# Kernel tuning notes

Measured on AMD Instinct MI355X. Metric: run time of the kernel, lower is better.

Reference implementation:

```python
import jax, jax.numpy as jnp
import numpy as np

N, E = 50000, 1600000            # nodes, edges
IN, H, OUT = 128, 128, 64        # in_channels, hidden_channels, out_channels
EPS = 1e-5                       # BatchNorm eps


def setup_inputs() -> dict:
    key = jax.random.key(0)
    ks = jax.random.split(key, 9)
    glorot = lambda k, shp, fan: jax.random.normal(k, shp, jnp.float32) * (1.0 / np.sqrt(fan))
    return {
        "x": jax.random.normal(ks[0], (N, IN), jnp.float32),
        "edge_index": jax.random.randint(ks[1], (2, E), 0, N),
        # layer 0: SAGEConv(IN, H) + BatchNorm(H)
        "Wl0": glorot(ks[2], (H, IN), IN), "Wr0": glorot(ks[3], (H, IN), IN),
        "b0": jnp.zeros((H,), jnp.float32),
        "g0": jnp.ones((H,), jnp.float32), "be0": jnp.zeros((H,), jnp.float32),
        # layer 1: SAGEConv(H, H) + BatchNorm(H)
        "Wl1": glorot(ks[4], (H, H), H), "Wr1": glorot(ks[5], (H, H), H),
        "b1": jnp.zeros((H,), jnp.float32),
        "g1": jnp.ones((H,), jnp.float32), "be1": jnp.zeros((H,), jnp.float32),
        # layer 2: SAGEConv(H, OUT)
        "Wl2": glorot(ks[6], (OUT, H), H), "Wr2": glorot(ks[7], (OUT, H), H),
        "b2": jnp.zeros((OUT,), jnp.float32),
    }


def _sage_conv(x, src, dst, Wl, Wr, b):
    """PyG SAGEConv with mean aggregation: lin_l(mean_{j->i} x_j) + lin_r(x_i) + b."""
    deg = jax.ops.segment_sum(jnp.ones((src.shape[0],), x.dtype), dst, num_segments=N)
    agg = jax.ops.segment_sum(x[src], dst, num_segments=N)  # [N, d] scatter-sum of gathered msgs
    agg = agg / jnp.maximum(deg, 1.0)[:, None]              # scatter-mean (0 for isolated nodes)
    return agg @ Wl.T + x @ Wr.T + b


def _batchnorm(x, gamma, beta):
    # training-mode BN over the node dimension (batch statistics)
    mu = jnp.mean(x, axis=0)
    var = jnp.var(x, axis=0)
    return (x - mu) * jax.lax.rsqrt(var + EPS) * gamma + beta


def reference(x, edge_index, Wl0, Wr0, b0, g0, be0, Wl1, Wr1, b1, g1, be1, Wl2, Wr2, b2):
    src, dst = edge_index[0], edge_index[1]
    h = jax.nn.relu(_batchnorm(_sage_conv(x, src, dst, Wl0, Wr0, b0), g0, be0))
    h = jax.nn.relu(_batchnorm(_sage_conv(h, src, dst, Wl1, Wr1, b1), g1, be1))
    return _sage_conv(h, src, dst, Wl2, Wr2, b2)
```

## Files before the change

### kernel.cpp

```cpp
#include <hip/hip_runtime.h>

#define NND 50000
#define NED 1600000
#define EPSBN 1e-5f
#define NB 196
#define EPB 8192
#define SCELEM (NB * NB)
#define SCPAD (38 * 1024)

typedef __attribute__((ext_vector_type(8))) short short8;
typedef __attribute__((ext_vector_type(4))) float f32x4;

__device__ __forceinline__ float bf_lo(unsigned u) {
    union { unsigned u; float f; } c; c.u = u << 16; return c.f;
}
__device__ __forceinline__ float bf_hi(unsigned u) {
    union { unsigned u; float f; } c; c.u = u & 0xffff0000u; return c.f;
}
__device__ __forceinline__ unsigned short f2b(float f) {
    union { float f; unsigned u; } c; c.f = f;
    unsigned r = (c.u + 0x7fffu + ((c.u >> 16) & 1u)) >> 16;
    return (unsigned short)r;
}

__global__ __launch_bounds__(256) void cast_bf16_kernel(const float* __restrict__ x,
                                                        unsigned short* __restrict__ xb) {
    int i = blockIdx.x * 256 + threadIdx.x;
    if (i >= NND * 16) return;
    const float4* p = (const float4*)x + (size_t)i * 2;
    float4 a = p[0], b = p[1];
    uint4 o;
    o.x = f2b(a.x) | ((unsigned)f2b(a.y) << 16);
    o.y = f2b(a.z) | ((unsigned)f2b(a.w) << 16);
    o.z = f2b(b.x) | ((unsigned)f2b(b.y) << 16);
    o.w = f2b(b.z) | ((unsigned)f2b(b.w) << 16);
    ((uint4*)xb)[i] = o;
}

__global__ __launch_bounds__(256) void eb_hist_kernel(const int* __restrict__ dst,
                                                      int* __restrict__ cntT) {
    __shared__ int hs[256];
    int t = threadIdx.x;
    hs[t] = 0;
    if (blockIdx.x == 0) {
        for (int i = t; i < SCPAD - SCELEM; i += 256) cntT[SCELEM + i] = 0;
    }
    __syncthreads();
    int base = blockIdx.x * EPB;
    for (int i = t; i < EPB; i += 256) {
        int e = base + i;
        if (e < NED) atomicAdd(&hs[dst[e] >> 8], 1);
    }
    __syncthreads();
    if (t < NB) cntT[t * NB + blockIdx.x] = hs[t];
}

__global__ __launch_bounds__(1024) void scan_p1_kernel(int* __restrict__ cnt,
                                                       int* __restrict__ psum) {
    __shared__ int s[1024];
    int t = threadIdx.x;
    int idx = blockIdx.x * 1024 + t;
    int v = cnt[idx];
    s[t] = v;
    __syncthreads();
    for (int o = 1; o < 1024; o <<= 1) {
        int a = (t >= o) ? s[t - o] : 0;
        __syncthreads();
        s[t] += a;
        __syncthreads();
    }
    cnt[idx] = s[t] - v;
    if (t == 1023) psum[blockIdx.x] = s[t];
}

__global__ __launch_bounds__(64) void scan_p2_kernel(int* __restrict__ psum,
                                                     int* __restrict__ binOff,
                                                     int* __restrict__ rowptr) {
    __shared__ int s[64];
    int t = threadIdx.x;
    int v = (t < 38) ? psum[t] : 0;
    s[t] = v;
    __syncthreads();
    for (int o = 1; o < 64; o <<= 1) {
        int a = (t >= o) ? s[t - o] : 0;
        __syncthreads();
        s[t] += a;
        __syncthreads();
    }
    if (t < 38) psum[t] = s[t] - v;
    if (t == 0) { binOff[NB] = NED; rowptr[NND] = NED; }
}

__global__ __launch_bounds__(1024) void scan_p3_kernel(int* __restrict__ cnt,
                                                       const int* __restrict__ psum,
                                                       int* __restrict__ binOff) {
    int idx = blockIdx.x * 1024 + threadIdx.x;
    int val = cnt[idx] + psum[blockIdx.x];
    cnt[idx] = val;
    int bin = idx / NB;
    if (bin < NB && idx - bin * NB == 0) binOff[bin] = val;
}

__global__ __launch_bounds__(256) void eb_scatter_kernel(const int* __restrict__ src,
                                                         const int* __restrict__ dst,
                                                         const int* __restrict__ offT,
                                                         unsigned* __restrict__ pairs) {
    __shared__ int cur[256];
    int t = threadIdx.x;
    if (t < NB) cur[t] = offT[t * NB + blockIdx.x];
    __syncthreads();
    int base = blockIdx.x * EPB;
    for (int i = t; i < EPB; i += 256) {
        int e = base + i;
        if (e < NED) {
            int d = dst[e];
            int pos = atomicAdd(&cur[d >> 8], 1);
            pairs[pos] = ((unsigned)src[e] << 8) | (unsigned)(d & 255);
        }
    }
}

__global__ __launch_bounds__(256) void bucket_finalize_kernel(const unsigned* __restrict__ pairs,
                                                              const int* __restrict__ binOff,
                                                              int* __restrict__ rowptr,
                                                              float* __restrict__ dinv,
                                                              int* __restrict__ csr) {
    __shared__ int hist[256], s[256], cur[256];
    int b = blockIdx.x, t = threadIdx.x;
    int beg = binOff[b], end = binOff[b + 1];
    hist[t] = 0;
    __syncthreads();
    for (int e = beg + t; e < end; e += 256)
        atomicAdd(&hist[pairs[e] & 255u], 1);
    __syncthreads();
    int v = hist[t];
    s[t] = v;
    __syncthreads();
#pragma unroll
    for (int o = 1; o < 256; o <<= 1) {
        int a = (t >= o) ? s[t - o] : 0;
        __syncthreads();
        s[t] += a;
        __syncthreads();
    }
    int base = beg + s[t] - v;
    int node = b * 256 + t;
    if (node < NND) {
        rowptr[node] = base;
        dinv[node] = 1.0f / (float)(v > 1 ? v : 1);
    }
    cur[t] = base;
    __syncthreads();
    for (int e = beg + t; e < end; e += 256) {
        unsigned p = pairs[e];
        int pos = atomicAdd(&cur[p & 255u], 1);
        csr[pos] = (int)(p >> 8);
    }
}

__global__ __launch_bounds__(256) void gather128_kernel(const unsigned short* __restrict__ xb,
                                                        const int* __restrict__ rowptr,
                                                        const int* __restrict__ csr,
                                                        const float* __restrict__ dinv,
                                                        unsigned short* __restrict__ aggb) {
    int w = threadIdx.x >> 6;
    int node = blockIdx.x * 4 + w;
    if (node >= NND) return;
    int lane = threadIdx.x & 63;
    int q = lane >> 4;
    int c8 = lane & 15;
    int beg = rowptr[node], end = rowptr[node + 1];
    const uint4* xv = (const uint4*)xb;

    float acc[8];
#pragma unroll
    for (int i = 0; i < 8; ++i) acc[i] = 0.f;

    for (int j = beg + q; j < end; j += 4) {
        int s = csr[j];
        uint4 v = xv[(size_t)s * 16 + c8];
        acc[0] += bf_lo(v.x); acc[1] += bf_hi(v.x);
        acc[2] += bf_lo(v.y); acc[3] += bf_hi(v.y);
        acc[4] += bf_lo(v.z); acc[5] += bf_hi(v.z);
        acc[6] += bf_lo(v.w); acc[7] += bf_hi(v.w);
    }
#pragma unroll
    for (int i = 0; i < 8; ++i) {
        acc[i] += __shfl_xor(acc[i], 16);
        acc[i] += __shfl_xor(acc[i], 32);
    }
    if (q == 0) {
        float dv = dinv[node];
        uint4 o;
        o.x = f2b(acc[0] * dv) | ((unsigned)f2b(acc[1] * dv) << 16);
        o.y = f2b(acc[2] * dv) | ((unsigned)f2b(acc[3] * dv) << 16);
        o.z = f2b(acc[4] * dv) | ((unsigned)f2b(acc[5] * dv) << 16);
        o.w = f2b(acc[6] * dv) | ((unsigned)f2b(acc[7] * dv) << 16);
        ((uint4*)aggb)[(size_t)node * 16 + c8] = o;
    }
}

__global__ __launch_bounds__(256) void gather64_kernel(const unsigned short* __restrict__ tb,
                                                       const int* __restrict__ rowptr,
                                                       const int* __restrict__ csr,
                                                       const float* __restrict__ dinv,
                                                       float* __restrict__ out) {
    int w = threadIdx.x >> 6;
    int node = blockIdx.x * 4 + w;
    if (node >= NND) return;
    int lane = threadIdx.x & 63;
    int g = lane >> 3;
    int c8 = lane & 7;
    int beg = rowptr[node], end = rowptr[node + 1];
    const uint4* tv = (const uint4*)tb;

    float acc[8];
#pragma unroll
    for (int i = 0; i < 8; ++i) acc[i] = 0.f;

    for (int j = beg + g; j < end; j += 8) {
        int s = csr[j];
        uint4 v = tv[(size_t)s * 8 + c8];
        acc[0] += bf_lo(v.x); acc[1] += bf_hi(v.x);
        acc[2] += bf_lo(v.y); acc[3] += bf_hi(v.y);
        acc[4] += bf_lo(v.z); acc[5] += bf_hi(v.z);
        acc[6] += bf_lo(v.w); acc[7] += bf_hi(v.w);
    }
#pragma unroll
    for (int i = 0; i < 8; ++i) {
        acc[i] += __shfl_xor(acc[i], 8);
        acc[i] += __shfl_xor(acc[i], 16);
        acc[i] += __shfl_xor(acc[i], 32);
    }
    if (g == 0) {
        float dv = dinv[node];
        float* po = out + (size_t)node * 64 + c8 * 8;
        float4 a = *(float4*)po, b = *(float4*)(po + 4);
        a.x += acc[0] * dv; a.y += acc[1] * dv; a.z += acc[2] * dv; a.w += acc[3] * dv;
        b.x += acc[4] * dv; b.y += acc[5] * dv; b.z += acc[6] * dv; b.w += acc[7] * dv;
        *(float4*)po = a; *(float4*)(po + 4) = b;
    }
}

__global__ __launch_bounds__(256) void pack_all_kernel(const float* __restrict__ Wl0,
                                                       const float* __restrict__ Wr0,
                                                       const float* __restrict__ Wl1,
                                                       const float* __restrict__ Wr1,
                                                       const float* __restrict__ Wl2,
                                                       const float* __restrict__ Wr2,
                                                       unsigned short* __restrict__ wp0,
                                                       unsigned short* __restrict__ wp1,
                                                       unsigned short* __restrict__ wp2,
                                                       float* __restrict__ stats) {
    int blk = blockIdx.x;
    if (blk == 0) { stats[threadIdx.x] = 0.f; stats[256 + threadIdx.x] = 0.f; }
    const float *Wl, *Wr; unsigned short* wp; bool l2f; int t;
    if (blk < 16)      { Wl = Wl0; Wr = Wr0; wp = wp0; l2f = false; t = blk * 256 + threadIdx.x; }
    else if (blk < 32) { Wl = Wl1; Wr = Wr1; wp = wp1; l2f = false; t = (blk - 16) * 256 + threadIdx.x; }
    else               { Wl = Wl2; Wr = Wr2; wp = wp2; l2f = true;  t = (blk - 32) * 256 + threadIdx.x; }
    int rem = t & 511;
    int ks = t >> 9;
    int cf = rem >> 6, l = rem & 63;
    int c = cf * 16 + (l & 15);
    int kb = ks * 32 + ((l >> 4) * 8);
    unsigned short v[8];
#pragma unroll
    for (int j = 0; j < 8; ++j) {
        int k = kb + j;
        float w;
        if (l2f) w = (c < 64) ? Wl[c * 128 + k] : Wr[(c - 64) * 128 + k];
        else     w = (k < 128) ? Wl[c * 128 + k] : Wr[c * 128 + (k - 128)];
        v[j] = f2b(w);
    }
    uint4 o;
    o.x = v[0] | ((unsigned)v[1] << 16);
    o.y = v[2] | ((unsigned)v[3] << 16);
    o.z = v[4] | ((unsigned)v[5] << 16);
    o.w = v[6] | ((unsigned)v[7] << 16);
    ((uint4*)wp)[t] = o;
}

template<int KS, int MODE>
__global__ __launch_bounds__(256) void gemm_mfma_kernel(const unsigned short* __restrict__ aggb,
                                                        const unsigned short* xinb,
                                                        const unsigned short* __restrict__ wpack,
                                                        const float* __restrict__ bias,
                                                        void* outv,
                                                        unsigned short* __restrict__ tbuf,
                                                        float* __restrict__ stats) {
    constexpr int NCF = 8, NCOL = 128;
    constexpr bool ST = (MODE == 0);
    __shared__ float o_s[64][NCOL + 4];
    __shared__ float sum_s[ST ? 4 : 1][ST ? 128 : 1];
    __shared__ float sq_s[ST ? 4 : 1][ST ? 128 : 1];

    const int t = threadIdx.x, wave = t >> 6, lane = t & 63;
    const int row0 = blockIdx.x * 64;
    const int arow = row0 + wave * 16 + (lane & 15);
    const bool avalid = arow < NND;
    const int ko = (lane >> 4) * 8;

    f32x4 acc[NCF];
#pragma unroll
    for (int cf = 0; cf < NCF; ++cf) acc[cf] = (f32x4){0.f, 0.f, 0.f, 0.f};

    const short8* wp = (const short8*)wpack;
#pragma unroll
    for (int ks = 0; ks < KS; ++ks) {
        short8 a = {0, 0, 0, 0, 0, 0, 0, 0};
        if (avalid) {
            int k = ks * 32 + ko;
            const unsigned short* base;
            if (MODE == 0)
                base = (k < 128) ? (aggb + (size_t)arow * 128 + k)
                                 : (xinb + (size_t)arow * 128 + (k - 128));
            else
                base = xinb + (size_t)arow * 128 + k;
            a = *(const short8*)base;
        }
#pragma unroll
        for (int cf = 0; cf < NCF; ++cf) {
            short8 b = wp[(ks * NCF + cf) * 64 + lane];
            acc[cf] = __builtin_amdgcn_mfma_f32_16x16x32_bf16(a, b, acc[cf], 0, 0, 0);
        }
    }

#pragma unroll
    for (int cf = 0; cf < NCF; ++cf)
#pragma unroll
        for (int r = 0; r < 4; ++r)
            o_s[wave * 16 + (lane >> 4) * 4 + r][cf * 16 + (lane & 15)] = acc[cf][r];

    if (ST) {
#pragma unroll
        for (int cf = 0; cf < NCF; ++cf) {
            float s = acc[cf][0] + acc[cf][1] + acc[cf][2] + acc[cf][3];
            float q = acc[cf][0] * acc[cf][0] + acc[cf][1] * acc[cf][1]
                    + acc[cf][2] * acc[cf][2] + acc[cf][3] * acc[cf][3];
            s += __shfl_xor(s, 16); s += __shfl_xor(s, 32);
            q += __shfl_xor(q, 16); q += __shfl_xor(q, 32);
            if (lane < 16) {
                sum_s[wave][cf * 16 + lane] = s;
                sq_s[wave][cf * 16 + lane] = q;
            }
        }
    }
    __syncthreads();

    const int r = t >> 2, q = t & 3;
    const int grow = row0 + r;
    if (grow < NND) {
        if (MODE == 0) {
            unsigned short* out = (unsigned short*)outv;
            const int c0 = q * 32;
#pragma unroll
            for (int g = 0; g < 4; ++g) {
                float v0 = o_s[r][c0 + g * 8 + 0], v1 = o_s[r][c0 + g * 8 + 1];
                float v2 = o_s[r][c0 + g * 8 + 2], v3 = o_s[r][c0 + g * 8 + 3];
                float v4 = o_s[r][c0 + g * 8 + 4], v5 = o_s[r][c0 + g * 8 + 5];
                float v6 = o_s[r][c0 + g * 8 + 6], v7 = o_s[r][c0 + g * 8 + 7];
                uint4 o;
                o.x = f2b(v0) | ((unsigned)f2b(v1) << 16);
                o.y = f2b(v2) | ((unsigned)f2b(v3) << 16);
                o.z = f2b(v4) | ((unsigned)f2b(v5) << 16);
                o.w = f2b(v6) | ((unsigned)f2b(v7) << 16);
                ((uint4*)(out + (size_t)grow * NCOL + c0))[g] = o;
            }
        } else {
            if (q < 2) {
                const int c0 = q * 32;
#pragma unroll
                for (int g = 0; g < 4; ++g) {
                    float v0 = o_s[r][c0 + g * 8 + 0], v1 = o_s[r][c0 + g * 8 + 1];
                    float v2 = o_s[r][c0 + g * 8 + 2], v3 = o_s[r][c0 + g * 8 + 3];
                    float v4 = o_s[r][c0 + g * 8 + 4], v5 = o_s[r][c0 + g * 8 + 5];
                    float v6 = o_s[r][c0 + g * 8 + 6], v7 = o_s[r][c0 + g * 8 + 7];
                    uint4 o;
                    o.x = f2b(v0) | ((unsigned)f2b(v1) << 16);
                    o.y = f2b(v2) | ((unsigned)f2b(v3) << 16);
                    o.z = f2b(v4) | ((unsigned)f2b(v5) << 16);
                    o.w = f2b(v6) | ((unsigned)f2b(v7) << 16);
                    ((uint4*)(tbuf + (size_t)grow * 64 + c0))[g] = o;
                }
            } else {
                float* out = (float*)outv;
                const int c0 = (q - 2) * 32;
#pragma unroll
                for (int g = 0; g < 8; ++g) {
                    float4 o;
                    o.x = o_s[r][64 + c0 + g * 4 + 0] + bias[c0 + g * 4 + 0];
                    o.y = o_s[r][64 + c0 + g * 4 + 1] + bias[c0 + g * 4 + 1];
                    o.z = o_s[r][64 + c0 + g * 4 + 2] + bias[c0 + g * 4 + 2];
                    o.w = o_s[r][64 + c0 + g * 4 + 3] + bias[c0 + g * 4 + 3];
                    ((float4*)(out + (size_t)grow * 64 + c0))[g] = o;
                }
            }
        }
    }

    if (ST && t < 128) {
        float s = sum_s[0][t] + sum_s[1][t] + sum_s[2][t] + sum_s[3][t];
        float q2 = sq_s[0][t] + sq_s[1][t] + sq_s[2][t] + sq_s[3][t];
        unsafeAtomicAdd(&stats[t], s);
        unsafeAtomicAdd(&stats[128 + t], q2);
    }
}

__global__ __launch_bounds__(256) void bn_relu_kernel(unsigned short* __restrict__ h,
                                                      const float* __restrict__ stats,
                                                      const float* __restrict__ gamma,
                                                      const float* __restrict__ beta) {
    __shared__ float ab_s[256];
    int t = threadIdx.x;
    if (t < 128) {
        float mu = stats[t] * (1.0f / NND);
        float var = stats[128 + t] * (1.0f / NND) - mu * mu;
        float rs = rsqrtf(var + EPSBN);
        float a = gamma[t] * rs;
        ab_s[t] = a;
        ab_s[128 + t] = beta[t] - mu * a;
    }
    __syncthreads();
    int i = blockIdx.x * 256 + t;
    if (i >= NND * 16) return;
    uint4 v = ((uint4*)h)[i];
    int c0 = (i & 15) * 8;
    float o[8] = {bf_lo(v.x), bf_hi(v.x), bf_lo(v.y), bf_hi(v.y),
                  bf_lo(v.z), bf_hi(v.z), bf_lo(v.w), bf_hi(v.w)};
#pragma unroll
    for (int j = 0; j < 8; ++j)
        o[j] = fmaxf(o[j] * ab_s[c0 + j] + ab_s[128 + c0 + j], 0.f);
    uint4 w;
    w.x = f2b(o[0]) | ((unsigned)f2b(o[1]) << 16);
    w.y = f2b(o[2]) | ((unsigned)f2b(o[3]) << 16);
    w.z = f2b(o[4]) | ((unsigned)f2b(o[5]) << 16);
    w.w = f2b(o[6]) | ((unsigned)f2b(o[7]) << 16);
    ((uint4*)h)[i] = w;
}

extern "C" void kernel_launch(void* const* d_in, const int* in_sizes, int n_in,
                              void* d_out, int out_size, void* d_ws, size_t ws_size,
                              hipStream_t stream) {
    const float* x   = (const float*)d_in[0];
    const int*   ei  = (const int*)d_in[1];
    const int* src = ei;
    const int* dst = ei + NED;
    const float* Wl0 = (const float*)d_in[2];
    const float* Wr0 = (const float*)d_in[3];
    const float* g0  = (const float*)d_in[5];
    const float* be0 = (const float*)d_in[6];
    const float* Wl1 = (const float*)d_in[7];
    const float* Wr1 = (const float*)d_in[8];
    const float* g1  = (const float*)d_in[10];
    const float* be1 = (const float*)d_in[11];
    const float* Wl2 = (const float*)d_in[12];
    const float* Wr2 = (const float*)d_in[13];
    const float* b2  = (const float*)d_in[14];
    float* out = (float*)d_out;

    const size_t NF = (size_t)NND * 128;
    unsigned short* aggb = (unsigned short*)d_ws;
    unsigned short* xb   = aggb + NF;
    unsigned short* h    = xb + NF;
    int*   csr    = (int*)(h + NF);
    float* dinv   = (float*)(csr + NED);
    int*   rowptr = (int*)(dinv + NND);
    int*   binOff = rowptr + NND + 8;
    int*   cntT   = binOff + 256;
    int*   psum   = cntT + SCPAD;
    unsigned short* wp0 = (unsigned short*)(psum + 64);
    unsigned short* wp1 = wp0 + 32768;
    unsigned short* wp2 = wp1 + 32768;
    float* stats  = (float*)(wp2 + 32768);
    unsigned* pairs = (unsigned*)aggb;

    const int GB = (NND + 3) / 4;
    const int GM = (NND + 63) / 64;

    cast_bf16_kernel<<<(NND * 16 + 255) / 256, 256, 0, stream>>>(x, xb);
    eb_hist_kernel<<<NB, 256, 0, stream>>>(dst, cntT);
    scan_p1_kernel<<<38, 1024, 0, stream>>>(cntT, psum);
    scan_p2_kernel<<<1, 64, 0, stream>>>(psum, binOff, rowptr);
    scan_p3_kernel<<<38, 1024, 0, stream>>>(cntT, psum, binOff);
    eb_scatter_kernel<<<NB, 256, 0, stream>>>(src, dst, cntT, pairs);
    bucket_finalize_kernel<<<NB, 256, 0, stream>>>(pairs, binOff, rowptr, dinv, csr);
    pack_all_kernel<<<40, 256, 0, stream>>>(Wl0, Wr0, Wl1, Wr1, Wl2, Wr2, wp0, wp1, wp2, stats);

    gather128_kernel<<<GB, 256, 0, stream>>>(xb, rowptr, csr, dinv, aggb);
    gemm_mfma_kernel<8, 0><<<GM, 256, 0, stream>>>(aggb, xb, wp0, nullptr, h, nullptr, stats);
    bn_relu_kernel<<<(NND * 16 + 255) / 256, 256, 0, stream>>>(h, stats, g0, be0);

    gather128_kernel<<<GB, 256, 0, stream>>>(h, rowptr, csr, dinv, aggb);
    gemm_mfma_kernel<8, 0><<<GM, 256, 0, stream>>>(aggb, h, wp1, nullptr, h, nullptr, stats + 256);
    bn_relu_kernel<<<(NND * 16 + 255) / 256, 256, 0, stream>>>(h, stats + 256, g1, be1);

    gemm_mfma_kernel<4, 2><<<GM, 256, 0, stream>>>(nullptr, h, wp2, b2, out, xb, nullptr);
    gather64_kernel<<<GB, 256, 0, stream>>>(xb, rowptr, csr, dinv, out);
}
```

Before: 438.0 us.

## Fuse neighbor mean-aggregation into layer GEMM via shared-memory staging

Replaces the separate gather128 and GEMM kernels for layers 0 and 1 with one kernel. Each block aggregates 64 nodes' neighbor features into shared memory as bf16, then runs the MFMA GEMM and BN statistics directly. This removes the global round-trip of the aggregated buffer and two launches. Layer 1 output is redirected to a new buffer because the gather reads all rows of its input. The trade-off is much less parallelism for the irregular gather: each wave serially processes 16 nodes, across far fewer blocks.

After: 484.8 us. 1.11x slower.

```diff
diff --git a/kernel.cpp b/kernel.cpp
--- a/kernel.cpp
+++ b/kernel.cpp
@@ -155,90 +155,6 @@
         unsigned p = pairs[e];
         int pos = atomicAdd(&cur[p & 255u], 1);
         csr[pos] = (int)(p >> 8);
-    }
-}
-
-__global__ __launch_bounds__(256) void gather128_kernel(const unsigned short* __restrict__ xb,
-                                                        const int* __restrict__ rowptr,
-                                                        const int* __restrict__ csr,
-                                                        const float* __restrict__ dinv,
-                                                        unsigned short* __restrict__ aggb) {
-    int w = threadIdx.x >> 6;
-    int node = blockIdx.x * 4 + w;
-    if (node >= NND) return;
-    int lane = threadIdx.x & 63;
-    int q = lane >> 4;
-    int c8 = lane & 15;
-    int beg = rowptr[node], end = rowptr[node + 1];
-    const uint4* xv = (const uint4*)xb;
-
-    float acc[8];
-#pragma unroll
-    for (int i = 0; i < 8; ++i) acc[i] = 0.f;
-
-    for (int j = beg + q; j < end; j += 4) {
-        int s = csr[j];
-        uint4 v = xv[(size_t)s * 16 + c8];
-        acc[0] += bf_lo(v.x); acc[1] += bf_hi(v.x);
-        acc[2] += bf_lo(v.y); acc[3] += bf_hi(v.y);
-        acc[4] += bf_lo(v.z); acc[5] += bf_hi(v.z);
-        acc[6] += bf_lo(v.w); acc[7] += bf_hi(v.w);
-    }
-#pragma unroll
-    for (int i = 0; i < 8; ++i) {
-        acc[i] += __shfl_xor(acc[i], 16);
-        acc[i] += __shfl_xor(acc[i], 32);
-    }
-    if (q == 0) {
-        float dv = dinv[node];
-        uint4 o;
-        o.x = f2b(acc[0] * dv) | ((unsigned)f2b(acc[1] * dv) << 16);
-        o.y = f2b(acc[2] * dv) | ((unsigned)f2b(acc[3] * dv) << 16);
-        o.z = f2b(acc[4] * dv) | ((unsigned)f2b(acc[5] * dv) << 16);
-        o.w = f2b(acc[6] * dv) | ((unsigned)f2b(acc[7] * dv) << 16);
-        ((uint4*)aggb)[(size_t)node * 16 + c8] = o;
-    }
-}
-
-__global__ __launch_bounds__(256) void gather64_kernel(const unsigned short* __restrict__ tb,
-                                                       const int* __restrict__ rowptr,
-                                                       const int* __restrict__ csr,
-                                                       const float* __restrict__ dinv,
-                                                       float* __restrict__ out) {
-    int w = threadIdx.x >> 6;
-    int node = blockIdx.x * 4 + w;
-    if (node >= NND) return;
-    int lane = threadIdx.x & 63;
-    int g = lane >> 3;
-    int c8 = lane & 7;
-    int beg = rowptr[node], end = rowptr[node + 1];
-    const uint4* tv = (const uint4*)tb;
-
-    float acc[8];
-#pragma unroll
-    for (int i = 0; i < 8; ++i) acc[i] = 0.f;
-
-    for (int j = beg + g; j < end; j += 8) {
-        int s = csr[j];
-        uint4 v = tv[(size_t)s * 8 + c8];
-        acc[0] += bf_lo(v.x); acc[1] += bf_hi(v.x);
-        acc[2] += bf_lo(v.y); acc[3] += bf_hi(v.y);
-        acc[4] += bf_lo(v.z); acc[5] += bf_hi(v.z);
-        acc[6] += bf_lo(v.w); acc[7] += bf_hi(v.w);
-    }
-#pragma unroll
-    for (int i = 0; i < 8; ++i) {
-        acc[i] += __shfl_xor(acc[i], 8);
-        acc[i] += __shfl_xor(acc[i], 16);
-        acc[i] += __shfl_xor(acc[i], 32);
-    }
-    if (g == 0) {
-        float dv = dinv[node];
-        float* po = out + (size_t)node * 64 + c8 * 8;
-        float4 a = *(float4*)po, b = *(float4*)(po + 4);
-        a.x += acc[0] * dv; a.y += acc[1] * dv; a.z += acc[2] * dv; a.w += acc[3] * dv;
-        b.x += acc[4] * dv; b.y += acc[5] * dv; b.z += acc[6] * dv; b.w += acc[7] * dv;
-        *(float4*)po = a; *(float4*)(po + 4) = b;
     }
 }
 
@@ -280,78 +196,172 @@
     ((uint4*)wp)[t] = o;
 }
 
-template<int KS, int MODE>
-__global__ __launch_bounds__(256) void gemm_mfma_kernel(const unsigned short* __restrict__ aggb,
-                                                        const unsigned short* xinb,
+union FSm {
+    unsigned short As[64][136];
+    struct {
+        float o_s[64][132];
+        float sum_s[4][128];
+        float sq_s[4][128];
+    } e;
+};
+
+__global__ __launch_bounds__(256) void fused_l01_kernel(const unsigned short* __restrict__ xb,
+                                                        const int* __restrict__ rowptr,
+                                                        const int* __restrict__ csr,
+                                                        const float* __restrict__ dinv,
                                                         const unsigned short* __restrict__ wpack,
-                                                        const float* __restrict__ bias,
-                                                        void* outv,
-                                                        unsigned short* __restrict__ tbuf,
+                                                        unsigned short* __restrict__ out,
                                                         float* __restrict__ stats) {
-    constexpr int NCF = 8, NCOL = 128;
-    constexpr bool ST = (MODE == 0);
-    __shared__ float o_s[64][NCOL + 4];
-    __shared__ float sum_s[ST ? 4 : 1][ST ? 128 : 1];
-    __shared__ float sq_s[ST ? 4 : 1][ST ? 128 : 1];
-
+    __shared__ FSm sm;
+    const int t = threadIdx.x, wave = t >> 6, lane = t & 63;
+    const int row0 = blockIdx.x * 64;
+    const int q = lane >> 4, c8 = lane & 15;
+    const uint4* xv = (const uint4*)xb;
+
+    for (int n = 0; n < 16; ++n) {
+        int node = row0 + wave * 16 + n;
+        if (node >= NND) break;
+        int beg = rowptr[node], end = rowptr[node + 1];
+        float acc[8];
+#pragma unroll
+        for (int i = 0; i < 8; ++i) acc[i] = 0.f;
+        for (int j = beg + q; j < end; j += 4) {
+            int s = csr[j];
+            uint4 v = xv[(size_t)s * 16 + c8];
+            acc[0] += bf_lo(v.x); acc[1] += bf_hi(v.x);
+            acc[2] += bf_lo(v.y); acc[3] += bf_hi(v.y);
+            acc[4] += bf_lo(v.z); acc[5] += bf_hi(v.z);
+            acc[6] += bf_lo(v.w); acc[7] += bf_hi(v.w);
+        }
+#pragma unroll
+        for (int i = 0; i < 8; ++i) {
+            acc[i] += __shfl_xor(acc[i], 16);
+            acc[i] += __shfl_xor(acc[i], 32);
+        }
+        if (q == 0) {
+            float dv = dinv[node];
+            uint4 o;
+            o.x = f2b(acc[0] * dv) | ((unsigned)f2b(acc[1] * dv) << 16);
+            o.y = f2b(acc[2] * dv) | ((unsigned)f2b(acc[3] * dv) << 16);
+            o.z = f2b(acc[4] * dv) | ((unsigned)f2b(acc[5] * dv) << 16);
+            o.w = f2b(acc[6] * dv) | ((unsigned)f2b(acc[7] * dv) << 16);
+            *(uint4*)&sm.As[wave * 16 + n][c8 * 8] = o;
+        }
+    }
+    __syncthreads();
+
+    const int arow = row0 + wave * 16 + (lane & 15);
+    const bool avalid = arow < NND;
+    const int ko = (lane >> 4) * 8;
+
+    f32x4 acc[8];
+#pragma unroll
+    for (int cf = 0; cf < 8; ++cf) acc[cf] = (f32x4){0.f, 0.f, 0.f, 0.f};
+
+    const short8* wp = (const short8*)wpack;
+#pragma unroll
+    for (int ks = 0; ks < 8; ++ks) {
+        short8 a = {0, 0, 0, 0, 0, 0, 0, 0};
+        if (avalid) {
+            if (ks < 4)
+                a = *(const short8*)&sm.As[wave * 16 + (lane & 15)][ks * 32 + ko];
+            else
+                a = *(const short8*)(xb + (size_t)arow * 128 + (ks - 4) * 32 + ko);
+        }
+#pragma unroll
+        for (int cf = 0; cf < 8; ++cf) {
+            short8 b = wp[(ks * 8 + cf) * 64 + lane];
+            acc[cf] = __builtin_amdgcn_mfma_f32_16x16x32_bf16(a, b, acc[cf], 0, 0, 0);
+        }
+    }
+    __syncthreads();
+
+#pragma unroll
+    for (int cf = 0; cf < 8; ++cf)
+#pragma unroll
+        for (int r = 0; r < 4; ++r)
+            sm.e.o_s[wave * 16 + (lane >> 4) * 4 + r][cf * 16 + (lane & 15)] = acc[cf][r];
+
+#pragma unroll
+    for (int cf = 0; cf < 8; ++cf) {
+        float s = acc[cf][0] + acc[cf][1] + acc[cf][2] + acc[cf][3];
+        float qq = acc[cf][0] * acc[cf][0] + acc[cf][1] * acc[cf][1]
+                 + acc[cf][2] * acc[cf][2] + acc[cf][3] * acc[cf][3];
+        s += __shfl_xor(s, 16); s += __shfl_xor(s, 32);
+        qq += __shfl_xor(qq, 16); qq += __shfl_xor(qq, 32);
+        if (lane < 16) {
+            sm.e.sum_s[wave][cf * 16 + lane] = s;
+            sm.e.sq_s[wave][cf * 16 + lane] = qq;
+        }
+    }
+    __syncthreads();
+
+    const int r = t >> 2, qc = t & 3;
+    const int grow = row0 + r;
+    if (grow < NND) {
+        const int c0 = qc * 32;
+#pragma unroll
+        for (int g = 0; g < 4; ++g) {
+            float v0 = sm.e.o_s[r][c0 + g * 8 + 0], v1 = sm.e.o_s[r][c0 + g * 8 + 1];
+            float v2 = sm.e.o_s[r][c0 + g * 8 + 2], v3 = sm.e.o_s[r][c0 + g * 8 + 3];
+            float v4 = sm.e.o_s[r][c0 + g * 8 + 4], v5 = sm.e.o_s[r][c0 + g * 8 + 5];
+            float v6 = sm.e.o_s[r][c0 + g * 8 + 6], v7 = sm.e.o_s[r][c0 + g * 8 + 7];
+            uint4 o;
+            o.x = f2b(v0) | ((unsigned)f2b(v1) << 16);
+            o.y = f2b(v2) | ((unsigned)f2b(v3) << 16);
+            o.z = f2b(v4) | ((unsigned)f2b(v5) << 16);
+            o.w = f2b(v6) | ((unsigned)f2b(v7) << 16);
+            ((uint4*)(out + (size_t)grow * 128 + c0))[g] = o;
+        }
+    }
+
+    if (t < 128) {
+        float s = sm.e.sum_s[0][t] + sm.e.sum_s[1][t] + sm.e.sum_s[2][t] + sm.e.sum_s[3][t];
+        float qq = sm.e.sq_s[0][t] + sm.e.sq_s[1][t] + sm.e.sq_s[2][t] + sm.e.sq_s[3][t];
+        unsafeAtomicAdd(&stats[t], s);
+        unsafeAtomicAdd(&stats[128 + t], qq);
+    }
+}
+
+__global__ __launch_bounds__(256) void gemm_l2_kernel(const unsigned short* __restrict__ xinb,
+                                                      const unsigned short* __restrict__ wpack,
+                                                      const float* __restrict__ bias,
+                                                      float* __restrict__ outf,
+                                                      unsigned short* __restrict__ tbuf) {
+    __shared__ float o_s[64][132];
     const int t = threadIdx.x, wave = t >> 6, lane = t & 63;
     const int row0 = blockIdx.x * 64;
     const int arow = row0 + wave * 16 + (lane & 15);
     const bool avalid = arow < NND;
     const int ko = (lane >> 4) * 8;
 
-    f32x4 acc[NCF];
-#pragma unroll
-    for (int cf = 0; cf < NCF; ++cf) acc[cf] = (f32x4){0.f, 0.f, 0.f, 0.f};
+    f32x4 acc[8];
+#pragma unroll
+    for (int cf = 0; cf < 8; ++cf) acc[cf] = (f32x4){0.f, 0.f, 0.f, 0.f};
 
     const short8* wp = (const short8*)wpack;
 #pragma unroll
-    for (int ks = 0; ks < KS; ++ks) {
+    for (int ks = 0; ks < 4; ++ks) {
         short8 a = {0, 0, 0, 0, 0, 0, 0, 0};
-        if (avalid) {
-            int k = ks * 32 + ko;
-            const unsigned short* base;
-            if (MODE == 0)
-                base = (k < 128) ? (aggb + (size_t)arow * 128 + k)
-                                 : (xinb + (size_t)arow * 128 + (k - 128));
-            else
-                base = xinb + (size_t)arow * 128 + k;
-            a = *(const short8*)base;
-        }
-#pragma unroll
-        for (int cf = 0; cf < NCF; ++cf) {
-            short8 b = wp[(ks * NCF + cf) * 64 + lane];
+        if (avalid) a = *(const short8*)(xinb + (size_t)arow * 128 + ks * 32 + ko);
+#pragma unroll
+        for (int cf = 0; cf < 8; ++cf) {
+            short8 b = wp[(ks * 8 + cf) * 64 + lane];
             acc[cf] = __builtin_amdgcn_mfma_f32_16x16x32_bf16(a, b, acc[cf], 0, 0, 0);
         }
     }
 
 #pragma unroll
-    for (int cf = 0; cf < NCF; ++cf)
+    for (int cf = 0; cf < 8; ++cf)
 #pragma unroll
         for (int r = 0; r < 4; ++r)
             o_s[wave * 16 + (lane >> 4) * 4 + r][cf * 16 + (lane & 15)] = acc[cf][r];
-
-    if (ST) {
-#pragma unroll
-        for (int cf = 0; cf < NCF; ++cf) {
-            float s = acc[cf][0] + acc[cf][1] + acc[cf][2] + acc[cf][3];
-            float q = acc[cf][0] * acc[cf][0] + acc[cf][1] * acc[cf][1]
-                    + acc[cf][2] * acc[cf][2] + acc[cf][3] * acc[cf][3];
-            s += __shfl_xor(s, 16); s += __shfl_xor(s, 32);
-            q += __shfl_xor(q, 16); q += __shfl_xor(q, 32);
-            if (lane < 16) {
-                sum_s[wave][cf * 16 + lane] = s;
-                sq_s[wave][cf * 16 + lane] = q;
-            }
-        }
-    }
     __syncthreads();
 
     const int r = t >> 2, q = t & 3;
     const int grow = row0 + r;
     if (grow < NND) {
-        if (MODE == 0) {
-            unsigned short* out = (unsigned short*)outv;
+        if (q < 2) {
             const int c0 = q * 32;
 #pragma unroll
             for (int g = 0; g < 4; ++g) {
@@ -364,45 +374,62 @@
                 o.y = f2b(v2) | ((unsigned)f2b(v3) << 16);
                 o.z = f2b(v4) | ((unsigned)f2b(v5) << 16);
                 o.w = f2b(v6) | ((unsigned)f2b(v7) << 16);
-                ((uint4*)(out + (size_t)grow * NCOL + c0))[g] = o;
+                ((uint4*)(tbuf + (size_t)grow * 64 + c0))[g] = o;
             }
         } else {
-            if (q < 2) {
-                const int c0 = q * 32;
-#pragma unroll
-                for (int g = 0; g < 4; ++g) {
-                    float v0 = o_s[r][c0 + g * 8 + 0], v1 = o_s[r][c0 + g * 8 + 1];
-                    float v2 = o_s[r][c0 + g * 8 + 2], v3 = o_s[r][c0 + g * 8 + 3];
-                    float v4 = o_s[r][c0 + g * 8 + 4], v5 = o_s[r][c0 + g * 8 + 5];
-                    float v6 = o_s[r][c0 + g * 8 + 6], v7 = o_s[r][c0 + g * 8 + 7];
-                    uint4 o;
-                    o.x = f2b(v0) | ((unsigned)f2b(v1) << 16);
-                    o.y = f2b(v2) | ((unsigned)f2b(v3) << 16);
-                    o.z = f2b(v4) | ((unsigned)f2b(v5) << 16);
-                    o.w = f2b(v6) | ((unsigned)f2b(v7) << 16);
-                    ((uint4*)(tbuf + (size_t)grow * 64 + c0))[g] = o;
-                }
-            } else {
-                float* out = (float*)outv;
-                const int c0 = (q - 2) * 32;
-#pragma unroll
-                for (int g = 0; g < 8; ++g) {
-                    float4 o;
-                    o.x = o_s[r][64 + c0 + g * 4 + 0] + bias[c0 + g * 4 + 0];
-                    o.y = o_s[r][64 + c0 + g * 4 + 1] + bias[c0 + g * 4 + 1];
-                    o.z = o_s[r][64 + c0 + g * 4 + 2] + bias[c0 + g * 4 + 2];
-                    o.w = o_s[r][64 + c0 + g * 4 + 3] + bias[c0 + g * 4 + 3];
-                    ((float4*)(out + (size_t)grow * 64 + c0))[g] = o;
-                }
+            const int c0 = (q - 2) * 32;
+#pragma unroll
+            for (int g = 0; g < 8; ++g) {
+                float4 o;
+                o.x = o_s[r][64 + c0 + g * 4 + 0] + bias[c0 + g * 4 + 0];
+                o.y = o_s[r][64 + c0 + g * 4 + 1] + bias[c0 + g * 4 + 1];
+                o.z = o_s[r][64 + c0 + g * 4 + 2] + bias[c0 + g * 4 + 2];
+                o.w = o_s[r][64 + c0 + g * 4 + 3] + bias[c0 + g * 4 + 3];
+                ((float4*)(outf + (size_t)grow * 64 + c0))[g] = o;
             }
         }
     }
-
-    if (ST && t < 128) {
-        float s = sum_s[0][t] + sum_s[1][t] + sum_s[2][t] + sum_s[3][t];
-        float q2 = sq_s[0][t] + sq_s[1][t] + sq_s[2][t] + sq_s[3][t];
-        unsafeAtomicAdd(&stats[t], s);
-        unsafeAtomicAdd(&stats[128 + t], q2);
+}
+
+__global__ __launch_bounds__(256) void gather64_kernel(const unsigned short* __restrict__ tb,
+                                                       const int* __restrict__ rowptr,
+                                                       const int* __restrict__ csr,
+                                                       const float* __restrict__ dinv,
+                                                       float* __restrict__ out) {
+    int w = threadIdx.x >> 6;
+    int node = blockIdx.x * 4 + w;
+    if (node >= NND) return;
+    int lane = threadIdx.x & 63;
+    int g = lane >> 3;
+    int c8 = lane & 7;
+    int beg = rowptr[node], end = rowptr[node + 1];
+    const uint4* tv = (const uint4*)tb;
+
+    float acc[8];
+#pragma unroll
+    for (int i = 0; i < 8; ++i) acc[i] = 0.f;
+
+    for (int j = beg + g; j < end; j += 8) {
+        int s = csr[j];
+        uint4 v = tv[(size_t)s * 8 + c8];
+        acc[0] += bf_lo(v.x); acc[1] += bf_hi(v.x);
+        acc[2] += bf_lo(v.y); acc[3] += bf_hi(v.y);
+        acc[4] += bf_lo(v.z); acc[5] += bf_hi(v.z);
+        acc[6] += bf_lo(v.w); acc[7] += bf_hi(v.w);
+    }
+#pragma unroll
+    for (int i = 0; i < 8; ++i) {
+        acc[i] += __shfl_xor(acc[i], 8);
+        acc[i] += __shfl_xor(acc[i], 16);
+        acc[i] += __shfl_xor(acc[i], 32);
+    }
+    if (g == 0) {
+        float dv = dinv[node];
+        float* po = out + (size_t)node * 64 + c8 * 8;
+        float4 a = *(float4*)po, b = *(float4*)(po + 4);
+        a.x += acc[0] * dv; a.y += acc[1] * dv; a.z += acc[2] * dv; a.w += acc[3] * dv;
+        b.x += acc[4] * dv; b.y += acc[5] * dv; b.z += acc[6] * dv; b.w += acc[7] * dv;
+        *(float4*)po = a; *(float4*)(po + 4) = b;
     }
 }
 
@@ -459,8 +486,8 @@
     float* out = (float*)d_out;
 
     const size_t NF = (size_t)NND * 128;
-    unsigned short* aggb = (unsigned short*)d_ws;
-    unsigned short* xb   = aggb + NF;
+    unsigned short* h2   = (unsigned short*)d_ws;
+    unsigned short* xb   = h2 + NF;
     unsigned short* h    = xb + NF;
     int*   csr    = (int*)(h + NF);
     float* dinv   = (float*)(csr + NED);
@@ -472,7 +499,7 @@
     unsigned short* wp1 = wp0 + 32768;
     unsigned short* wp2 = wp1 + 32768;
     float* stats  = (float*)(wp2 + 32768);
-    unsigned* pairs = (unsigned*)aggb;
+    unsigned* pairs = (unsigned*)h2;
 
     const int GB = (NND + 3) / 4;
     const int GM = (NND + 63) / 64;
@@ -486,14 +513,12 @@
     bucket_finalize_kernel<<<NB, 256, 0, stream>>>(pairs, binOff, rowptr, dinv, csr);
     pack_all_kernel<<<40, 256, 0, stream>>>(Wl0, Wr0, Wl1, Wr1, Wl2, Wr2, wp0, wp1, wp2, stats);
 
-    gather128_kernel<<<GB, 256, 0, stream>>>(xb, rowptr, csr, dinv, aggb);
-    gemm_mfma_kernel<8, 0><<<GM, 256, 0, stream>>>(aggb, xb, wp0, nullptr, h, nullptr, stats);
+    fused_l01_kernel<<<GM, 256, 0, stream>>>(xb, rowptr, csr, dinv, wp0, h, stats);
     bn_relu_kernel<<<(NND * 16 + 255) / 256, 256, 0, stream>>>(h, stats, g0, be0);
 
-    gather128_kernel<<<GB, 256, 0, stream>>>(h, rowptr, csr, dinv, aggb);
-    gemm_mfma_kernel<8, 0><<<GM, 256, 0, stream>>>(aggb, h, wp1, nullptr, h, nullptr, stats + 256);
-    bn_relu_kernel<<<(NND * 16 + 255) / 256, 256, 0, stream>>>(h, stats + 256, g1, be1);
-
-    gemm_mfma_kernel<4, 2><<<GM, 256, 0, stream>>>(nullptr, h, wp2, b2, out, xb, nullptr);
+    fused_l01_kernel<<<GM, 256, 0, stream>>>(h, rowptr, csr, dinv, wp1, h2, stats + 256);
+    bn_relu_kernel<<<(NND * 16 + 255) / 256, 256, 0, stream>>>(h2, stats + 256, g1, be1);
+
+    gemm_l2_kernel<<<GM, 256, 0, stream>>>(h2, wp2, b2, out, xb);
     gather64_kernel<<<GB, 256, 0, stream>>>(xb, rowptr, csr, dinv, out);
 }
```
